# Optimization experiments

Hardware: AMD Instinct MI355X
Metric: run time of the kernel (lower is better)

## Reference

```python
import jax, jax.numpy as jnp
import numpy as np

B, H, W, C = 2, 64, 64, 96
DIN, NST, RNK, K = 192, 16, 6, 4
L = H * W


def _make_ids():
    idx = np.arange(L).reshape(H, W)
    p0 = idx.reshape(-1)
    p1 = idx.T.reshape(-1)
    p2 = p0[::-1].copy()
    p3 = p1[::-1].copy()
    scan = np.stack([p0, p1, p2, p3]).astype(np.int32)
    inv = np.stack([np.argsort(p) for p in scan]).astype(np.int32)
    return jnp.asarray(scan), jnp.asarray(inv)


def setup_inputs() -> dict:
    key = jax.random.key(0)
    ks = jax.random.split(key, 10)
    scan_ids, inv_ids = _make_ids()
    std = RNK ** -0.5
    # dt bias init: inverse-softplus of dt ~ LogUniform(1e-3, 1e-1), as in VMM.dt_init
    u = jax.random.uniform(ks[5], (K, DIN))
    dt = jnp.exp(u * (np.log(0.1) - np.log(0.001)) + np.log(0.001))
    dt_b = dt + jnp.log(-jnp.expm1(-dt))
    return {
        "x": jax.random.normal(ks[0], (B, H, W, C), jnp.float32),
        "W_in": jax.random.normal(ks[1], (2 * DIN, C), jnp.float32) * 0.02,
        "conv_w": jax.random.normal(ks[2], (DIN, 1, 3, 3), jnp.float32) * 0.1,
        "conv_b": jnp.zeros((DIN,), jnp.float32),
        "x_proj_w": jax.random.normal(ks[3], (K, RNK + 2 * NST, DIN), jnp.float32) * 0.02,
        "dt_w": jax.random.uniform(ks[4], (K, DIN, RNK), jnp.float32, -std, std),
        "dt_b": dt_b.astype(jnp.float32),
        "A_logs": jnp.log(jnp.tile(jnp.arange(1, NST + 1, dtype=jnp.float32)[None], (K * DIN, 1))),
        "Ds": jnp.ones((K * DIN,), jnp.float32),
        "gate_w": jax.random.normal(ks[6], (4 * DIN, 4), jnp.float32) * 0.1,  # grouped 1x1 conv, groups=DIN
        "gate_b": jnp.zeros((4 * DIN,), jnp.float32),
        "ln_g": jnp.ones((DIN,), jnp.float32),
        "ln_b": jnp.zeros((DIN,), jnp.float32),
        "W_out": jax.random.normal(ks[7], (C, DIN), jnp.float32) * 0.02,
        "scan_ids": scan_ids,
        "inv_ids": inv_ids,
    }


def _forward(x, W_in, conv_w, conv_b, x_proj_w, dt_w, dt_b, A_logs, Ds, gate_w, gate_b, ln_g, ln_b, W_out, scan_ids, inv_ids):
    b, h, w, c = x.shape
    l = h * w
    din = conv_w.shape[0]
    k = x_proj_w.shape[0]
    nst = A_logs.shape[1]
    rnk = dt_w.shape[2]
    # in_proj + split into x / gate z
    xz = x @ W_in.T
    xc, z = jnp.split(xz, 2, axis=-1)
    xc = jnp.transpose(xc, (0, 3, 1, 2))  # (b, din, h, w)
    # depthwise 3x3 conv + SiLU
    xc = jax.lax.conv_general_dilated(
        xc, conv_w, (1, 1), "SAME", feature_group_count=din,
        dimension_numbers=("NCHW", "OIHW", "NCHW")) + conv_b[None, :, None, None]
    xc = jax.nn.silu(xc)
    # multi-directional gather (mair_ids_scan)
    xf = xc.reshape(b, din, l)
    xs = jnp.moveaxis(xf[:, :, scan_ids], 2, 1)  # (b, k, din, l)
    # x_proj (grouped 1x1 conv) -> dt, B, C
    x_dbl = jnp.einsum("bkdl,krd->bkrl", xs, x_proj_w)
    dts, Bs, Cs = jnp.split(x_dbl, [rnk, rnk + nst], axis=2)  # (b,k,rnk,l),(b,k,n,l),(b,k,n,l)
    delta = jax.nn.softplus(jnp.einsum("bkrl,kdr->bkdl", dts, dt_w) + dt_b[None, :, :, None])
    A = -jnp.exp(A_logs).reshape(k, din, nst)
    dA = jnp.exp(delta[..., None] * A[None, :, :, None, :])              # (b,k,d,l,n)
    dBu = (delta * xs)[..., None] * jnp.moveaxis(Bs, 2, 3)[:, :, None]   # (b,k,d,l,n)

    def step(hst, inp):
        da, dbu = inp
        hst = da * hst + dbu
        return hst, hst

    h0 = jnp.zeros((b, k, din, nst), jnp.float32)
    _, hs = jax.lax.scan(step, h0, (jnp.moveaxis(dA, 3, 0), jnp.moveaxis(dBu, 3, 0)))  # (l,b,k,d,n)
    ys = jnp.einsum("lbkdn,bknl->bkdl", hs, Cs) + xs * Ds.reshape(k, din)[None, :, :, None]
    # inverse scatter (mair_ids_inverse) + concat along channels
    y = jax.vmap(lambda yk, ik: yk[..., ik], in_axes=(1, 0), out_axes=1)(ys, inv_ids)
    y = y.reshape(b, k * din, h, w)
    # ShuffleAttn gating: group = din, group_channels = k
    shuf = y.reshape(b, k, din, h, w).transpose(0, 2, 1, 3, 4).reshape(b, k * din, h, w)
    pooled = shuf.mean(axis=(2, 3)).reshape(b, din, k)
    gate = jax.nn.sigmoid(jnp.einsum("bgi,goi->bgo", pooled, gate_w.reshape(din, k, k)) + gate_b.reshape(din, k))
    gate = gate.transpose(0, 2, 1).reshape(b, k * din)  # channel_rearrange
    y = y * gate[:, :, None, None]
    # sum the 4 direction branches
    y = y.reshape(b, k, din, h, w).sum(axis=1)
    y = jnp.transpose(y, (0, 2, 3, 1))  # (b,h,w,din)
    # LayerNorm(d_inner)
    mu = y.mean(-1, keepdims=True)
    var = ((y - mu) ** 2).mean(-1, keepdims=True)
    y = (y - mu) / jnp.sqrt(var + 1e-5) * ln_g + ln_b
    y = y * jax.nn.silu(z)
    return y @ W_out.T


def reference(x, W_in, conv_w, conv_b, x_proj_w, dt_w, dt_b, A_logs, Ds, gate_w, gate_b, ln_g, ln_b, W_out, scan_ids, inv_ids):
    return _forward(x, W_in, conv_w, conv_b, x_proj_w, dt_w, dt_b, A_logs, Ds, gate_w, gate_b, ln_g, ln_b, W_out, scan_ids, inv_ids)
```

## Files before the change

### kernel.cpp

```cpp
#include <hip/hip_runtime.h>
#include <math.h>

#define BB 2
#define CC 96
#define DIN 192
#define NST 16
#define RNK 6
#define KK 4
#define LL 4096
#define RTOT (RNK + 2*NST)


__global__ __launch_bounds__(256) void k_inproj(const float* __restrict__ x,
        const float* __restrict__ W_in, float* __restrict__ xc_pre,
        float* __restrict__ z_silu) {
    __shared__ float lx[96*33];
    __shared__ float wt[48*196];
    int b = blockIdx.y, z = blockIdx.z;
    int l0 = blockIdx.x * 32;
    int t = threadIdx.x;
    for (int i = 0; i < 3; ++i) {
        int e4 = t + 256*i;
        int c4 = e4 % 24, l = e4 / 24;
        float4 v = *(const float4*)&x[((size_t)(b*LL + l0 + l))*96 + 4*c4];
        lx[(4*c4+0)*33 + l] = v.x;
        lx[(4*c4+1)*33 + l] = v.y;
        lx[(4*c4+2)*33 + l] = v.z;
        lx[(4*c4+3)*33 + l] = v.w;
    }
    int lg = t & 7;
    int og = t >> 3;
    float acc[4][6];
    #pragma unroll
    for (int j = 0; j < 4; ++j)
        #pragma unroll
        for (int q = 0; q < 6; ++q) acc[j][q] = 0.f;
    for (int p = 0; p < 2; ++p) {
        __syncthreads();
        for (int i = 0; i < 9; ++i) {
            int e4 = t + 256*i;
            int cc4 = e4 % 12, oc = e4 / 12;
            float4 v = *(const float4*)&W_in[((size_t)(z*192 + oc))*96 + p*48 + 4*cc4];
            wt[(4*cc4+0)*196 + oc] = v.x;
            wt[(4*cc4+1)*196 + oc] = v.y;
            wt[(4*cc4+2)*196 + oc] = v.z;
            wt[(4*cc4+3)*196 + oc] = v.w;
        }
        __syncthreads();
        #pragma unroll 4
        for (int cc = 0; cc < 48; ++cc) {
            int c = p*48 + cc;
            float x0 = lx[c*33 + 4*lg + 0];
            float x1 = lx[c*33 + 4*lg + 1];
            float x2 = lx[c*33 + 4*lg + 2];
            float x3 = lx[c*33 + 4*lg + 3];
            const float* wr = &wt[cc*196 + 6*og];
            float2 w0 = *(const float2*)(wr);
            float2 w1 = *(const float2*)(wr + 2);
            float2 w2 = *(const float2*)(wr + 4);
            float wv[6] = {w0.x,w0.y, w1.x,w1.y, w2.x,w2.y};
            #pragma unroll
            for (int q = 0; q < 6; ++q) {
                acc[0][q] += x0*wv[q];
                acc[1][q] += x1*wv[q];
                acc[2][q] += x2*wv[q];
                acc[3][q] += x3*wv[q];
            }
        }
    }
    float* dst = (z == 0) ? xc_pre : z_silu;
    #pragma unroll
    for (int j = 0; j < 4; ++j) {
        int l = l0 + 4*lg + j;
        size_t base = (size_t)(b*LL + l)*DIN + 6*og;
        float v[6];
        #pragma unroll
        for (int q = 0; q < 6; ++q) {
            float a = acc[j][q];
            v[q] = z ? a/(1.f + __expf(-a)) : a;
        }
        *(float2*)&dst[base]     = make_float2(v[0], v[1]);
        *(float2*)&dst[base + 2] = make_float2(v[2], v[3]);
        *(float2*)&dst[base + 4] = make_float2(v[4], v[5]);
    }
}

__global__ __launch_bounds__(256) void k_conv(const float* __restrict__ xc,
        const float* __restrict__ cw, const float* __restrict__ cb,
        float* __restrict__ out, float* __restrict__ outT) {
    int gid = blockIdx.x*256 + threadIdx.x;
    int dq = gid % 48;
    int r = gid / 48;
    int l = r & 4095, b = r >> 12;
    int w = l & 63, h = l >> 6;
    int d0 = dq*4;
    float4 acc = *(const float4*)&cb[d0];
    float wreg[4][9];
    #pragma unroll
    for (int j = 0; j < 4; ++j)
        #pragma unroll
        for (int tp = 0; tp < 9; ++tp) wreg[j][tp] = cw[(d0+j)*9 + tp];
    #pragma unroll
    for (int dh = -1; dh <= 1; ++dh) {
        int h2 = h + dh;
        bool okh = (h2 >= 0) && (h2 < 64);
        #pragma unroll
        for (int dw = -1; dw <= 1; ++dw) {
            int w2 = w + dw;
            if (okh && w2 >= 0 && w2 < 64) {
                float4 v = *(const float4*)&xc[((size_t)(b*LL + h2*64 + w2))*DIN + d0];
                int tp = (dh+1)*3 + (dw+1);
                acc.x += v.x*wreg[0][tp];
                acc.y += v.y*wreg[1][tp];
                acc.z += v.z*wreg[2][tp];
                acc.w += v.w*wreg[3][tp];
            }
        }
    }
    float4 o;
    o.x = acc.x/(1.f + __expf(-acc.x));
    o.y = acc.y/(1.f + __expf(-acc.y));
    o.z = acc.z/(1.f + __expf(-acc.z));
    o.w = acc.w/(1.f + __expf(-acc.w));
    *(float4*)&out[((size_t)(b*LL + l))*DIN + d0] = o;
    int lt = w*64 + h;
    *(float4*)&outT[((size_t)(b*LL + lt))*DIN + d0] = o;
}

__global__ __launch_bounds__(512) void k_proj(const float* __restrict__ xconv,
        const float* __restrict__ xconvT, const float* __restrict__ xpw,
        float* __restrict__ dts, float* __restrict__ Bs, float* __restrict__ Cs) {
    __shared__ float lxs[96*65];
    __shared__ float lw[RTOT*96];
    __shared__ float lbc[64*33];
    int k = blockIdx.y, b = blockIdx.z;
    int l0 = blockIdx.x * 64;
    int t = threadIdx.x;
    const float* src = (k & 1) ? xconvT : xconv;
    int rb = (k < 2) ? l0 : (LL - 1 - l0);
    int rs = (k < 2) ? 1 : -1;
    int l = t & 63;
    int rg = __builtin_amdgcn_readfirstlane(t >> 6);
    float acc[5];
    #pragma unroll
    for (int j = 0; j < 5; ++j) acc[j] = 0.f;
    for (int p = 0; p < 2; ++p) {
        __syncthreads();
        for (int i = 0; i < 3; ++i) {
            int e4 = t + 512*i;
            int dd4 = e4 % 24, ll = e4 / 24;
            int row = rb + rs*ll;
            float4 v = *(const float4*)&src[((size_t)(b*LL + row))*DIN + p*96 + 4*dd4];
            lxs[(4*dd4+0)*65 + ll] = v.x;
            lxs[(4*dd4+1)*65 + ll] = v.y;
            lxs[(4*dd4+2)*65 + ll] = v.z;
            lxs[(4*dd4+3)*65 + ll] = v.w;
        }
        for (int i = 0; i < 2; ++i) {
            int e4 = t + 512*i;
            if (e4 < RTOT*24) {
                int r = e4 / 24, dd4 = e4 % 24;
                *(float4*)&lw[r*96 + 4*dd4] =
                    *(const float4*)&xpw[(size_t)k*RTOT*DIN + r*DIN + p*96 + 4*dd4];
            }
        }
        __syncthreads();
        for (int dd = 0; dd < 96; dd += 4) {
            float x0 = lxs[(dd+0)*65 + l];
            float x1 = lxs[(dd+1)*65 + l];
            float x2 = lxs[(dd+2)*65 + l];
            float x3 = lxs[(dd+3)*65 + l];
            #pragma unroll
            for (int j = 0; j < 5; ++j) {
                int r = rg + 8*j;
                if (r < RTOT) {
                    float4 w = *(const float4*)&lw[r*96 + dd];
                    acc[j] += x0*w.x + x1*w.y + x2*w.z + x3*w.w;
                }
            }
        }
    }
    int bk = b*KK + k;
    #pragma unroll
    for (int j = 0; j < 5; ++j) {
        int r = rg + 8*j;
        if (r < RNK)       dts[((size_t)bk*LL + l0 + l)*8 + r] = acc[j];
        else if (r < RTOT) lbc[l*33 + (r - RNK)] = acc[j];
    }
    __syncthreads();
    size_t rowb = ((size_t)bk*LL + l0)*NST;
    for (int i = 0; i < 2; ++i) {
        int e = t + 512*i;
        int n = e & 15, ll = e >> 4;
        Bs[rowb + ll*NST + n] = lbc[ll*33 + n];
        Cs[rowb + ll*NST + n] = lbc[ll*33 + 16 + n];
    }
}

__global__ __launch_bounds__(384) void k_scan1(const float* __restrict__ xconv,
        const float* __restrict__ xconvT,
        const float* __restrict__ Bs, const float* __restrict__ Cs,
        const float* __restrict__ dts, const float* __restrict__ dtw,
        const float* __restrict__ dtb,
        const float* __restrict__ A_logs, const float* __restrict__ Ds,
        float* __restrict__ y_scan, float* __restrict__ segA,
        float* __restrict__ segB, int SL) {
    int seg = blockIdx.x, bk = blockIdx.y;
    int b = bk >> 2, k = bk & 3;
    int t = threadIdx.x;
    int half = t & 1, d = t >> 1;
    int l0 = seg * SL;
    const float* src = (k & 1) ? xconvT : xconv;
    int rb = (k < 2) ? l0 : (LL - 1 - l0);
    int rs = (k < 2) ? 1 : -1;
    float Av[8];
    {
        const float4* ap = (const float4*)(A_logs + ((k*DIN + d)*NST + half*8));
        float4 a0 = ap[0], a1 = ap[1];
        Av[0]=-__expf(a0.x); Av[1]=-__expf(a0.y); Av[2]=-__expf(a0.z); Av[3]=-__expf(a0.w);
        Av[4]=-__expf(a1.x); Av[5]=-__expf(a1.y); Av[6]=-__expf(a1.z); Av[7]=-__expf(a1.w);
    }
    float Av0 = -__expf(A_logs[(k*DIN + d)*NST]);
    bool okl = true;
    #pragma unroll
    for (int q = 0; q < 8; ++q) {
        float m = (float)(half*8 + q + 1);
        okl = okl && (fabsf(Av[q] - m*Av0) <= 1e-4f*m);
    }
    int fast = __all(okl);
    float Dv = Ds[k*DIN + d];
    float wdt[RNK];
    float bdt = dtb[k*DIN + d];
    #pragma unroll
    for (int r = 0; r < RNK; ++r) wdt[r] = dtw[(k*DIN + d)*RNK + r];
    float h[8];
    #pragma unroll
    for (int n = 0; n < 8; ++n) h[n] = 0.f;
    float sumdv = 0.f;
    const float* dbase = dts + ((size_t)bk*LL + l0)*8;
    const float* bbase = Bs + ((size_t)bk*LL + l0)*NST + half*8;
    const float* cbase = Cs + ((size_t)bk*LL + l0)*NST + half*8;
    float xn = src[((size_t)(b*LL + rb))*DIN + d];
    float drc[RNK];
    #pragma unroll
    for (int r = 0; r < RNK; ++r) drc[r] = dbase[r];
    float4 bn0 = *(const float4*)bbase,      bn1 = *(const float4*)(bbase + 4);
    float4 cn0 = *(const float4*)cbase,      cn1 = *(const float4*)(cbase + 4);
    if (fast) {
        for (int li = 0; li < SL; ++li) {
            float xv = xn;
            float drv[RNK];
            #pragma unroll
            for (int r = 0; r < RNK; ++r) drv[r] = drc[r];
            float4 b0 = bn0, b1 = bn1, c0v = cn0, c1v = cn1;
            if (li + 1 < SL) {
                int row = rb + rs*(li + 1);
                xn = src[((size_t)(b*LL + row))*DIN + d];
                #pragma unroll
                for (int r = 0; r < RNK; ++r) drc[r] = dbase[(li+1)*8 + r];
                bn0 = *(const float4*)(bbase + (size_t)(li+1)*NST);
                bn1 = *(const float4*)(bbase + (size_t)(li+1)*NST + 4);
                cn0 = *(const float4*)(cbase + (size_t)(li+1)*NST);
                cn1 = *(const float4*)(cbase + (size_t)(li+1)*NST + 4);
            }
            float aa = bdt;
            #pragma unroll
            for (int r = 0; r < RNK; ++r) aa += drv[r]*wdt[r];
            float dv = fmaxf(aa, 0.f) + __logf(1.f + __expf(-fabsf(aa)));
            sumdv += dv;
            float dxv = dv * xv;
            float bb[8] = {b0.x,b0.y,b0.z,b0.w, b1.x,b1.y,b1.z,b1.w};
            float cc[8] = {c0v.x,c0v.y,c0v.z,c0v.w, c1v.x,c1v.y,c1v.z,c1v.w};
            float E  = __expf(dv * Av0);
            float E2 = E*E, E4 = E2*E2;
            float P[8];
            P[0] = E;      P[1] = E2;     P[2] = E2*E;    P[3] = E4;
            P[4] = E4*E;   P[5] = E4*E2;  P[6] = E4*P[2]; P[7] = E4*E4;
            float s = half ? P[7] : 1.0f;
            float y = 0.f;
            #pragma unroll
            for (int n = 0; n < 8; ++n) {
                h[n] = (s*P[n])*h[n] + dxv*bb[n];
                y += h[n]*cc[n];
            }
            y += __shfl_xor(y, 1);
            if (half == 0) {
                y += xv * Dv;
                y_scan[((size_t)(bk*LL + l0 + li))*DIN + d] = y;
            }
        }
    } else {
        for (int li = 0; li < SL; ++li) {
            float xv = xn;
            float drv[RNK];
            #pragma unroll
            for (int r = 0; r < RNK; ++r) drv[r] = drc[r];
            float4 b0 = bn0, b1 = bn1, c0v = cn0, c1v = cn1;
            if (li + 1 < SL) {
                int row = rb + rs*(li + 1);
                xn = src[((size_t)(b*LL + row))*DIN + d];
                #pragma unroll
                for (int r = 0; r < RNK; ++r) drc[r] = dbase[(li+1)*8 + r];
                bn0 = *(const float4*)(bbase + (size_t)(li+1)*NST);
                bn1 = *(const float4*)(bbase + (size_t)(li+1)*NST + 4);
                cn0 = *(const float4*)(cbase + (size_t)(li+1)*NST);
                cn1 = *(const float4*)(cbase + (size_t)(li+1)*NST + 4);
            }
            float aa = bdt;
            #pragma unroll
            for (int r = 0; r < RNK; ++r) aa += drv[r]*wdt[r];
            float dv = fmaxf(aa, 0.f) + __logf(1.f + __expf(-fabsf(aa)));
            sumdv += dv;
            float dxv = dv * xv;
            float bb[8] = {b0.x,b0.y,b0.z,b0.w, b1.x,b1.y,b1.z,b1.w};
            float cc[8] = {c0v.x,c0v.y,c0v.z,c0v.w, c1v.x,c1v.y,c1v.z,c1v.w};
            float y = 0.f;
            #pragma unroll
            for (int n = 0; n < 8; ++n) {
                float e2 = __expf(dv * Av[n]);
                h[n] = e2*h[n] + dxv*bb[n];
                y += h[n]*cc[n];
            }
            y += __shfl_xor(y, 1);
            if (half == 0) {
                y += xv * Dv;
                y_scan[((size_t)(bk*LL + l0 + li))*DIN + d] = y;
            }
        }
    }
    float a[8];
    #pragma unroll
    for (int n = 0; n < 8; ++n) a[n] = __expf(Av[n]*sumdv);
    size_t base = (((size_t)bk*gridDim.x + seg)*DIN + d)*NST + half*8;
    *(float4*)&segA[base]     = make_float4(a[0],a[1],a[2],a[3]);
    *(float4*)&segA[base + 4] = make_float4(a[4],a[5],a[6],a[7]);
    *(float4*)&segB[base]     = make_float4(h[0],h[1],h[2],h[3]);
    *(float4*)&segB[base + 4] = make_float4(h[4],h[5],h[6],h[7]);
}

__global__ __launch_bounds__(256) void k_scan2(const float* segA,
        const float* segB, float* hinit, float* poolsum, int SEGC) {
    int idx = blockIdx.x*256 + threadIdx.x;
    if (idx < BB*DIN*KK) poolsum[idx] = 0.f;
    if (idx >= BB*KK*DIN*NST) return;
    int bk = idx / (DIN*NST);
    int dn = idx % (DIN*NST);
    const size_t stride = DIN*NST;
    size_t o = (size_t)bk*SEGC*stride + dn;
    float h = 0.f;
    for (int s = 0; s < SEGC; s += 8) {
        float av[8], bv[8];
        #pragma unroll
        for (int j = 0; j < 8; ++j) {
            av[j] = segA[o + j*stride];
            bv[j] = segB[o + j*stride];
        }
        #pragma unroll
        for (int j = 0; j < 8; ++j) {
            hinit[o + j*stride] = h;
            h = av[j]*h + bv[j];
        }
        o += 8*stride;
    }
}

__global__ __launch_bounds__(384) void k_apply(const float* __restrict__ Cs,
        const float* __restrict__ dts, const float* __restrict__ dtw,
        const float* __restrict__ dtb,
        const float* __restrict__ A_logs, const float* __restrict__ hinit,
        float* __restrict__ y_scan, float* __restrict__ poolsum, int SL) {
    int seg = blockIdx.x, bk = blockIdx.y;
    int b = bk >> 2, k = bk & 3;
    int t = threadIdx.x;
    int half = t & 1, d = t >> 1;
    int l0 = seg * SL;
    float Av[8];
    {
        const float4* ap = (const float4*)(A_logs + ((k*DIN + d)*NST + half*8));
        float4 a0 = ap[0], a1 = ap[1];
        Av[0]=-__expf(a0.x); Av[1]=-__expf(a0.y); Av[2]=-__expf(a0.z); Av[3]=-__expf(a0.w);
        Av[4]=-__expf(a1.x); Av[5]=-__expf(a1.y); Av[6]=-__expf(a1.z); Av[7]=-__expf(a1.w);
    }
    float Av0 = -__expf(A_logs[(k*DIN + d)*NST]);
    bool okl = true;
    #pragma unroll
    for (int q = 0; q < 8; ++q) {
        float m = (float)(half*8 + q + 1);
        okl = okl && (fabsf(Av[q] - m*Av0) <= 1e-4f*m);
    }
    int fast = __all(okl);
    float h0[8];
    {
        size_t base = (((size_t)bk*gridDim.x + seg)*DIN + d)*NST + half*8;
        float4 v0 = *(const float4*)&hinit[base];
        float4 v1 = *(const float4*)&hinit[base + 4];
        h0[0]=v0.x; h0[1]=v0.y; h0[2]=v0.z; h0[3]=v0.w;
        h0[4]=v1.x; h0[5]=v1.y; h0[6]=v1.z; h0[7]=v1.w;
    }
    float wdt[RNK];
    float bdt = dtb[k*DIN + d];
    #pragma unroll
    for (int r = 0; r < RNK; ++r) wdt[r] = dtw[(k*DIN + d)*RNK + r];
    float cum = 0.f;
    float pool = 0.f;
    const float* dbase = dts + ((size_t)bk*LL + l0)*8;
    const float* cbase = Cs + ((size_t)bk*LL + l0)*NST + half*8;
    float drc[RNK];
    #pragma unroll
    for (int r = 0; r < RNK; ++r) drc[r] = dbase[r];
    float4 cn0 = *(const float4*)cbase, cn1 = *(const float4*)(cbase + 4);
    for (int li = 0; li < SL; ++li) {
        float drv[RNK];
        #pragma unroll
        for (int r = 0; r < RNK; ++r) drv[r] = drc[r];
        float4 c0v = cn0, c1v = cn1;
        if (li + 1 < SL) {
            #pragma unroll
            for (int r = 0; r < RNK; ++r) drc[r] = dbase[(li+1)*8 + r];
            cn0 = *(const float4*)(cbase + (size_t)(li+1)*NST);
            cn1 = *(const float4*)(cbase + (size_t)(li+1)*NST + 4);
        }
        float aa = bdt;
        #pragma unroll
        for (int r = 0; r < RNK; ++r) aa += drv[r]*wdt[r];
        cum += fmaxf(aa, 0.f) + __logf(1.f + __expf(-fabsf(aa)));
        float cc[8] = {c0v.x,c0v.y,c0v.z,c0v.w, c1v.x,c1v.y,c1v.z,c1v.w};
        float g;
        if (fast) {
            float E = __expf(Av0 * cum);
            g = 0.f;
            #pragma unroll
            for (int q = 7; q >= 0; --q) g = g*E + cc[q]*h0[q];
            g *= E;
            if (half) {
                float E2 = E*E, E4 = E2*E2;
                g *= E4*E4;
            }
        } else {
            g = 0.f;
            #pragma unroll
            for (int q = 0; q < 8; ++q)
                g += cc[q]*h0[q]*__expf(Av[q]*cum);
        }
        g += __shfl_xor(g, 1);
        if (half == 0) {
            size_t yo = ((size_t)(bk*LL + l0 + li))*DIN + d;
            float y = y_scan[yo] + g;
            y_scan[yo] = y;
            pool += y;
        }
    }
    if (half == 0) atomicAdd(&poolsum[(b*DIN + d)*KK + k], pool);
}

__global__ __launch_bounds__(256) void k_final(const float* __restrict__ y_scan,
        const float* __restrict__ poolsum, const float* __restrict__ gw,
        const float* __restrict__ gb, const float* __restrict__ z_silu,
        const float* __restrict__ lng, const float* __restrict__ lnb,
        const float* __restrict__ Wout, float* __restrict__ out) {
    __shared__ float buf[16*196];
    __shared__ float lgate[DIN*KK];
    __shared__ float lwout[96*100];
    __shared__ float lmu[16], lrs[16];
    int b = blockIdx.y;
    int l0 = blockIdx.x * 16;
    int t = threadIdx.x;
    for (int e = t; e < DIN*KK; e += 256) {
        int d = e >> 2, o = e & 3;
        float acc = gb[d*KK + o];
        #pragma unroll
        for (int i = 0; i < KK; ++i)
            acc += (poolsum[(b*DIN + d)*KK + i] * (1.f/LL)) * gw[(d*KK + o)*KK + i];
        lgate[d*KK + o] = 1.f/(1.f + __expf(-acc));
    }
    __syncthreads();
    for (int i = 0; i < 3; ++i) {
        int e4 = t + 256*i;
        int d4 = e4 % 48, l = e4 / 48;
        int db = 4*d4;
        int ls = l0 + l;
        int tpl = ((ls & 63) << 6) | (ls >> 6);
        int pk[4] = {ls, tpl, LL - 1 - ls, LL - 1 - tpl};
        float4 acc = make_float4(0.f, 0.f, 0.f, 0.f);
        #pragma unroll
        for (int k = 0; k < KK; ++k) {
            float4 v = *(const float4*)&y_scan[((size_t)((b*KK + k)*LL + pk[k]))*DIN + db];
            acc.x += v.x * lgate[(db+0)*KK + k];
            acc.y += v.y * lgate[(db+1)*KK + k];
            acc.z += v.z * lgate[(db+2)*KK + k];
            acc.w += v.w * lgate[(db+3)*KK + k];
        }
        *(float4*)&buf[l*196 + db] = acc;
    }
    __syncthreads();
    int l2 = t >> 4, q = t & 15;
    float s = 0.f, s2 = 0.f;
    for (int i = 0; i < 12; ++i) {
        float v = buf[l2*196 + q + 16*i];
        s += v; s2 += v*v;
    }
    s += __shfl_xor(s, 1);  s2 += __shfl_xor(s2, 1);
    s += __shfl_xor(s, 2);  s2 += __shfl_xor(s2, 2);
    s += __shfl_xor(s, 4);  s2 += __shfl_xor(s2, 4);
    s += __shfl_xor(s, 8);  s2 += __shfl_xor(s2, 8);
    if (q == 0) {
        float mu = s * (1.f/DIN);
        float var = s2 * (1.f/DIN) - mu*mu;
        lmu[l2] = mu;
        lrs[l2] = rsqrtf(var + 1e-5f);
    }
    __syncthreads();
    for (int i = 0; i < 3; ++i) {
        int e4 = t + 256*i;
        int d4 = e4 % 48, l = e4 / 48;
        int db = 4*d4;
        float4 v  = *(float4*)&buf[l*196 + db];
        float4 g4 = *(const float4*)&lng[db];
        float4 b4 = *(const float4*)&lnb[db];
        float4 z4 = *(const float4*)&z_silu[((size_t)(b*LL + l0 + l))*DIN + db];
        float mu = lmu[l], rs = lrs[l];
        v.x = ((v.x - mu)*rs*g4.x + b4.x) * z4.x;
        v.y = ((v.y - mu)*rs*g4.y + b4.y) * z4.y;
        v.z = ((v.z - mu)*rs*g4.z + b4.z) * z4.z;
        v.w = ((v.w - mu)*rs*g4.w + b4.w) * z4.w;
        *(float4*)&buf[l*196 + db] = v;
    }
    int l = t & 15;
    int c0 = (t >> 4) * 6;
    float acc[6];
    #pragma unroll
    for (int cc = 0; cc < 6; ++cc) acc[cc] = 0.f;
    for (int p = 0; p < 2; ++p) {
        __syncthreads();
        for (int i = 0; i < 9; ++i) {
            int e4 = t + 256*i;
            int dd4 = e4 % 24, cc = e4 / 24;
            *(float4*)&lwout[cc*100 + 4*dd4] =
                *(const float4*)&Wout[(size_t)cc*DIN + p*96 + 4*dd4];
        }
        __syncthreads();
        for (int d4 = 0; d4 < 24; ++d4) {
            float4 v = *(float4*)&buf[l*196 + p*96 + 4*d4];
            #pragma unroll
            for (int cc = 0; cc < 6; ++cc) {
                float4 w = *(const float4*)&lwout[(c0 + cc)*100 + 4*d4];
                acc[cc] += v.x*w.x + v.y*w.y + v.z*w.z + v.w*w.w;
            }
        }
    }
    #pragma unroll
    for (int cc = 0; cc < 6; ++cc)
        out[((size_t)(b*LL + l0 + l))*CC + c0 + cc] = acc[cc];
}

extern "C" void kernel_launch(void* const* d_in, const int* in_sizes, int n_in,
                              void* d_out, int out_size, void* d_ws, size_t ws_size,
                              hipStream_t stream) {
    const float* x      = (const float*)d_in[0];
    const float* W_in   = (const float*)d_in[1];
    const float* conv_w = (const float*)d_in[2];
    const float* conv_b = (const float*)d_in[3];
    const float* xpw    = (const float*)d_in[4];
    const float* dt_w   = (const float*)d_in[5];
    const float* dt_b   = (const float*)d_in[6];
    const float* A_logs = (const float*)d_in[7];
    const float* Ds     = (const float*)d_in[8];
    const float* gate_w = (const float*)d_in[9];
    const float* gate_b = (const float*)d_in[10];
    const float* ln_g   = (const float*)d_in[11];
    const float* ln_b   = (const float*)d_in[12];
    const float* W_out  = (const float*)d_in[13];
    float* out = (float*)d_out;

    const size_t baseF = 6291456ull + 3ull*1572864 + 262144ull + 2ull*524288 + 3072;
    int SEGC = 16;
    if ((baseF + 2ull*128*24576)*4 <= ws_size) SEGC = 128;
    else if ((baseF + 2ull*64*24576)*4 <= ws_size) SEGC = 64;
    else if ((baseF + 2ull*32*24576)*4 <= ws_size) SEGC = 32;
    int SL = LL / SEGC;
    size_t segF = (size_t)SEGC * 24576;

    float* ws      = (float*)d_ws;
    float* y_scan  = ws;
    float* xc_pre  = ws;
    float* z_silu  = y_scan  + 6291456;
    float* xconv   = z_silu  + 1572864;
    float* xconvT  = xconv   + 1572864;
    float* dts     = xconvT  + 1572864;
    float* Bs      = dts     + 262144;
    float* Cs      = Bs      + 524288;
    float* poolsum = Cs      + 524288;
    float* segA    = poolsum + 3072;
    float* segB    = segA    + segF;
    float* hinit   = segA;

    k_inproj<<<dim3(LL/32, BB, 2), 256, 0, stream>>>(x, W_in, xc_pre, z_silu);
    k_conv<<<(BB*LL*48)/256, 256, 0, stream>>>(xc_pre, conv_w, conv_b,
                                               xconv, xconvT);
    k_proj<<<dim3(LL/64, KK, BB), 512, 0, stream>>>(xconv, xconvT, xpw,
                                                    dts, Bs, Cs);
    k_scan1<<<dim3(SEGC, BB*KK), 384, 0, stream>>>(xconv, xconvT, Bs, Cs, dts,
                                                   dt_w, dt_b, A_logs, Ds,
                                                   y_scan, segA, segB, SL);
    k_scan2<<<(BB*KK*DIN*NST + 255)/256, 256, 0, stream>>>(segA, segB, hinit,
                                                           poolsum, SEGC);
    k_apply<<<dim3(SEGC, BB*KK), 384, 0, stream>>>(Cs, dts, dt_w, dt_b,
                                                   A_logs, hinit,
                                                   y_scan, poolsum, SL);
    k_final<<<dim3(LL/16, BB), 256, 0, stream>>>(y_scan, poolsum, gate_w, gate_b,
                                                 z_silu, ln_g, ln_b, W_out, out);
}
```

Measured before the change: 282.6 us.

## Stage scan B/C/dt chunks in shared memory and coalesce y_scan stores

Both scan kernels now process the segment in 32-step chunks. The block cooperatively loads the B, C and dt rows for each chunk into shared memory, so threads stop issuing redundant per-thread global loads. y_scan values are gathered in shared memory and written, or read and written, as coalesced float4 rows instead of strided scalar accesses. This adds several syncthreads per chunk and more LDS use, and it drops the register prefetch pipelining. It also assumes SL is a multiple of 32.

```diff
diff --git a/kernel.cpp b/kernel.cpp
--- a/kernel.cpp
+++ b/kernel.cpp
@@ -205,6 +205,10 @@
         const float* __restrict__ A_logs, const float* __restrict__ Ds,
         float* __restrict__ y_scan, float* __restrict__ segA,
         float* __restrict__ segB, int SL) {
+    __shared__ float sB[32*NST];
+    __shared__ float sC[32*NST];
+    __shared__ float sD[32*8];
+    __shared__ float sY[32*DIN];
     int seg = blockIdx.x, bk = blockIdx.y;
     int b = bk >> 2, k = bk & 3;
     int t = threadIdx.x;
@@ -237,96 +241,73 @@
     #pragma unroll
     for (int n = 0; n < 8; ++n) h[n] = 0.f;
     float sumdv = 0.f;
-    const float* dbase = dts + ((size_t)bk*LL + l0)*8;
-    const float* bbase = Bs + ((size_t)bk*LL + l0)*NST + half*8;
-    const float* cbase = Cs + ((size_t)bk*LL + l0)*NST + half*8;
     float xn = src[((size_t)(b*LL + rb))*DIN + d];
-    float drc[RNK];
-    #pragma unroll
-    for (int r = 0; r < RNK; ++r) drc[r] = dbase[r];
-    float4 bn0 = *(const float4*)bbase,      bn1 = *(const float4*)(bbase + 4);
-    float4 cn0 = *(const float4*)cbase,      cn1 = *(const float4*)(cbase + 4);
-    if (fast) {
-        for (int li = 0; li < SL; ++li) {
+    for (int c0 = 0; c0 < SL; c0 += 32) {
+        if (t < 128) {
+            *(float4*)&sB[4*t] =
+                *(const float4*)&Bs[((size_t)bk*LL + l0 + c0)*NST + 4*t];
+        } else if (t < 256) {
+            int u = t - 128;
+            *(float4*)&sC[4*u] =
+                *(const float4*)&Cs[((size_t)bk*LL + l0 + c0)*NST + 4*u];
+        } else if (t < 320) {
+            int u = t - 256;
+            *(float4*)&sD[4*u] =
+                *(const float4*)&dts[((size_t)bk*LL + l0 + c0)*8 + 4*u];
+        }
+        __syncthreads();
+        for (int li2 = 0; li2 < 32; ++li2) {
+            int li = c0 + li2;
             float xv = xn;
-            float drv[RNK];
-            #pragma unroll
-            for (int r = 0; r < RNK; ++r) drv[r] = drc[r];
-            float4 b0 = bn0, b1 = bn1, c0v = cn0, c1v = cn1;
             if (li + 1 < SL) {
                 int row = rb + rs*(li + 1);
                 xn = src[((size_t)(b*LL + row))*DIN + d];
-                #pragma unroll
-                for (int r = 0; r < RNK; ++r) drc[r] = dbase[(li+1)*8 + r];
-                bn0 = *(const float4*)(bbase + (size_t)(li+1)*NST);
-                bn1 = *(const float4*)(bbase + (size_t)(li+1)*NST + 4);
-                cn0 = *(const float4*)(cbase + (size_t)(li+1)*NST);
-                cn1 = *(const float4*)(cbase + (size_t)(li+1)*NST + 4);
             }
             float aa = bdt;
             #pragma unroll
-            for (int r = 0; r < RNK; ++r) aa += drv[r]*wdt[r];
+            for (int r = 0; r < RNK; ++r) aa += sD[li2*8 + r]*wdt[r];
             float dv = fmaxf(aa, 0.f) + __logf(1.f + __expf(-fabsf(aa)));
             sumdv += dv;
             float dxv = dv * xv;
-            float bb[8] = {b0.x,b0.y,b0.z,b0.w, b1.x,b1.y,b1.z,b1.w};
-            float cc[8] = {c0v.x,c0v.y,c0v.z,c0v.w, c1v.x,c1v.y,c1v.z,c1v.w};
-            float E  = __expf(dv * Av0);
-            float E2 = E*E, E4 = E2*E2;
-            float P[8];
-            P[0] = E;      P[1] = E2;     P[2] = E2*E;    P[3] = E4;
-            P[4] = E4*E;   P[5] = E4*E2;  P[6] = E4*P[2]; P[7] = E4*E4;
-            float s = half ? P[7] : 1.0f;
-            float y = 0.f;
-            #pragma unroll
-            for (int n = 0; n < 8; ++n) {
-                h[n] = (s*P[n])*h[n] + dxv*bb[n];
-                y += h[n]*cc[n];
-            }
-            y += __shfl_xor(y, 1);
-            if (half == 0) {
-                y += xv * Dv;
-                y_scan[((size_t)(bk*LL + l0 + li))*DIN + d] = y;
-            }
-        }
-    } else {
-        for (int li = 0; li < SL; ++li) {
-            float xv = xn;
-            float drv[RNK];
-            #pragma unroll
-            for (int r = 0; r < RNK; ++r) drv[r] = drc[r];
-            float4 b0 = bn0, b1 = bn1, c0v = cn0, c1v = cn1;
-            if (li + 1 < SL) {
-                int row = rb + rs*(li + 1);
-                xn = src[((size_t)(b*LL + row))*DIN + d];
-                #pragma unroll
-                for (int r = 0; r < RNK; ++r) drc[r] = dbase[(li+1)*8 + r];
-                bn0 = *(const float4*)(bbase + (size_t)(li+1)*NST);
-                bn1 = *(const float4*)(bbase + (size_t)(li+1)*NST + 4);
-                cn0 = *(const float4*)(cbase + (size_t)(li+1)*NST);
-                cn1 = *(const float4*)(cbase + (size_t)(li+1)*NST + 4);
-            }
-            float aa = bdt;
-            #pragma unroll
-            for (int r = 0; r < RNK; ++r) aa += drv[r]*wdt[r];
-            float dv = fmaxf(aa, 0.f) + __logf(1.f + __expf(-fabsf(aa)));
-            sumdv += dv;
-            float dxv = dv * xv;
+            float4 b0 = *(const float4*)&sB[li2*NST + half*8];
+            float4 b1 = *(const float4*)&sB[li2*NST + half*8 + 4];
+            float4 c0v = *(const float4*)&sC[li2*NST + half*8];
+            float4 c1v = *(const float4*)&sC[li2*NST + half*8 + 4];
             float bb[8] = {b0.x,b0.y,b0.z,b0.w, b1.x,b1.y,b1.z,b1.w};
             float cc[8] = {c0v.x,c0v.y,c0v.z,c0v.w, c1v.x,c1v.y,c1v.z,c1v.w};
             float y = 0.f;
-            #pragma unroll
-            for (int n = 0; n < 8; ++n) {
-                float e2 = __expf(dv * Av[n]);
-                h[n] = e2*h[n] + dxv*bb[n];
-                y += h[n]*cc[n];
+            if (fast) {
+                float E  = __expf(dv * Av0);
+                float E2 = E*E, E4 = E2*E2;
+                float P[8];
+                P[0] = E;      P[1] = E2;     P[2] = E2*E;    P[3] = E4;
+                P[4] = E4*E;   P[5] = E4*E2;  P[6] = E4*P[2]; P[7] = E4*E4;
+                float s = half ? P[7] : 1.0f;
+                #pragma unroll
+                for (int n = 0; n < 8; ++n) {
+                    h[n] = (s*P[n])*h[n] + dxv*bb[n];
+                    y += h[n]*cc[n];
+                }
+            } else {
+                #pragma unroll
+                for (int n = 0; n < 8; ++n) {
+                    float e2 = __expf(dv * Av[n]);
+                    h[n] = e2*h[n] + dxv*bb[n];
+                    y += h[n]*cc[n];
+                }
             }
             y += __shfl_xor(y, 1);
             if (half == 0) {
-                y += xv * Dv;
-                y_scan[((size_t)(bk*LL + l0 + li))*DIN + d] = y;
-            }
-        }
+                sY[li2*DIN + d] = y + xv * Dv;
+            }
+        }
+        __syncthreads();
+        size_t ybase = ((size_t)bk*LL + l0 + c0)*DIN;
+        for (int i = 0; i < 4; ++i) {
+            int e4 = t + 384*i;
+            *(float4*)&y_scan[ybase + 4*e4] = *(const float4*)&sY[4*e4];
+        }
+        __syncthreads();
     }
     float a[8];
     #pragma unroll
@@ -369,6 +350,9 @@
         const float* __restrict__ dtb,
         const float* __restrict__ A_logs, const float* __restrict__ hinit,
         float* __restrict__ y_scan, float* __restrict__ poolsum, int SL) {
+    __shared__ float sC[32*NST];
+    __shared__ float sD[32*8];
+    __shared__ float sY[32*DIN];
     int seg = blockIdx.x, bk = blockIdx.y;
     int b = bk >> 2, k = bk & 3;
     int t = threadIdx.x;
@@ -403,52 +387,59 @@
     for (int r = 0; r < RNK; ++r) wdt[r] = dtw[(k*DIN + d)*RNK + r];
     float cum = 0.f;
     float pool = 0.f;
-    const float* dbase = dts + ((size_t)bk*LL + l0)*8;
-    const float* cbase = Cs + ((size_t)bk*LL + l0)*NST + half*8;
-    float drc[RNK];
-    #pragma unroll
-    for (int r = 0; r < RNK; ++r) drc[r] = dbase[r];
-    float4 cn0 = *(const float4*)cbase, cn1 = *(const float4*)(cbase + 4);
-    for (int li = 0; li < SL; ++li) {
-        float drv[RNK];
-        #pragma unroll
-        for (int r = 0; r < RNK; ++r) drv[r] = drc[r];
-        float4 c0v = cn0, c1v = cn1;
-        if (li + 1 < SL) {
+    for (int c0 = 0; c0 < SL; c0 += 32) {
+        if (t < 128) {
+            *(float4*)&sC[4*t] =
+                *(const float4*)&Cs[((size_t)bk*LL + l0 + c0)*NST + 4*t];
+        } else if (t < 192) {
+            int u = t - 128;
+            *(float4*)&sD[4*u] =
+                *(const float4*)&dts[((size_t)bk*LL + l0 + c0)*8 + 4*u];
+        }
+        size_t ybase = ((size_t)bk*LL + l0 + c0)*DIN;
+        for (int i = 0; i < 4; ++i) {
+            int e4 = t + 384*i;
+            *(float4*)&sY[4*e4] = *(const float4*)&y_scan[ybase + 4*e4];
+        }
+        __syncthreads();
+        for (int li2 = 0; li2 < 32; ++li2) {
+            float aa = bdt;
             #pragma unroll
-            for (int r = 0; r < RNK; ++r) drc[r] = dbase[(li+1)*8 + r];
-            cn0 = *(const float4*)(cbase + (size_t)(li+1)*NST);
-            cn1 = *(const float4*)(cbase + (size_t)(li+1)*NST + 4);
-        }
-        float aa = bdt;
-        #pragma unroll
-        for (int r = 0; r < RNK; ++r) aa += drv[r]*wdt[r];
-        cum += fmaxf(aa, 0.f) + __logf(1.f + __expf(-fabsf(aa)));
-        float cc[8] = {c0v.x,c0v.y,c0v.z,c0v.w, c1v.x,c1v.y,c1v.z,c1v.w};
-        float g;
-        if (fast) {
-            float E = __expf(Av0 * cum);
-            g = 0.f;
-            #pragma unroll
-            for (int q = 7; q >= 0; --q) g = g*E + cc[q]*h0[q];
-            g *= E;
-            if (half) {
-                float E2 = E*E, E4 = E2*E2;
-                g *= E4*E4;
-            }
-        } else {
-            g = 0.f;
-            #pragma unroll
-            for (int q = 0; q < 8; ++q)
-                g += cc[q]*h0[q]*__expf(Av[q]*cum);
-        }
-        g += __shfl_xor(g, 1);
-        if (half == 0) {
-            size_t yo = ((size_t)(bk*LL + l0 + li))*DIN + d;
-            float y = y_scan[yo] + g;
-            y_scan[yo] = y;
-            pool += y;
-        }
+            for (int r = 0; r < RNK; ++r) aa += sD[li2*8 + r]*wdt[r];
+            cum += fmaxf(aa, 0.f) + __logf(1.f + __expf(-fabsf(aa)));
+            float4 c0v = *(const float4*)&sC[li2*NST + half*8];
+            float4 c1v = *(const float4*)&sC[li2*NST + half*8 + 4];
+            float cc[8] = {c0v.x,c0v.y,c0v.z,c0v.w, c1v.x,c1v.y,c1v.z,c1v.w};
+            float g;
+            if (fast) {
+                float E = __expf(Av0 * cum);
+                g = 0.f;
+                #pragma unroll
+                for (int q = 7; q >= 0; --q) g = g*E + cc[q]*h0[q];
+                g *= E;
+                if (half) {
+                    float E2 = E*E, E4 = E2*E2;
+                    g *= E4*E4;
+                }
+            } else {
+                g = 0.f;
+                #pragma unroll
+                for (int q = 0; q < 8; ++q)
+                    g += cc[q]*h0[q]*__expf(Av[q]*cum);
+            }
+            g += __shfl_xor(g, 1);
+            if (half == 0) {
+                float y = sY[li2*DIN + d] + g;
+                sY[li2*DIN + d] = y;
+                pool += y;
+            }
+        }
+        __syncthreads();
+        for (int i = 0; i < 4; ++i) {
+            int e4 = t + 384*i;
+            *(float4*)&y_scan[ybase + 4*e4] = *(const float4*)&sY[4*e4];
+        }
+        __syncthreads();
     }
     if (half == 0) atomicAdd(&poolsum[(b*DIN + d)*KK + k], pool);
 }
```

New measurement: 265.0 us. 6.2% less time.
